# Performance work log

Measured on AMD Instinct MI355X. Metric: run time of the kernel, lower is better.

Reference implementation:

```python
import jax, jax.numpy as jnp
import numpy as np

CENTER_EXTEND_PX = 3.0  # center_extend_px
SIGMA = 2.0             # center_gt_blur
KSIZE = 21              # GaussianLayer: ReflectionPad2d(10) + 21x21 depthwise gaussian
PAD = KSIZE // 2


def _gaussian_kernel():
    ax = np.arange(KSIZE, dtype=np.float64) - PAD
    xx, yy = np.meshgrid(ax, ax)
    g = np.exp(-(xx ** 2 + yy ** 2) / (2.0 * SIGMA ** 2))
    g /= g.sum()
    return jnp.asarray(g, dtype=jnp.float32)


def _blur(x, kernel):
    # x: [H, W]; reflect-pad then VALID depthwise conv == GaussianLayer
    xp = jnp.pad(x, PAD, mode='reflect')
    return jax.lax.conv_general_dilated(xp[None, None], kernel[None, None], (1, 1), 'VALID')[0, 0]


def setup_inputs():
    key = jax.random.key(0)
    B, N, H, W = 4, 64, 512, 512
    kc = jax.random.fold_in(key, 1)
    # centers[b, n] = (y, x) pixel coordinates; >0 means valid
    centers = jax.random.randint(kc, (B, N, 2), 1, min(H, W)).astype(jnp.float32)
    centerdir_gt = jnp.zeros((B, 6, H, W), dtype=jnp.float32)
    return {"centers": centers, "centerdir_gt": centerdir_gt, "kernel": _gaussian_kernel()}


def reference(centers, centerdir_gt, kernel):
    B, _, H, W = centerdir_gt.shape
    # xym grid: xym[0] varies along width, xym[1] varies along height (integer coords)
    grid_h = jnp.arange(H, dtype=jnp.float32)[:, None]  # xym[1]: [H,1]
    grid_w = jnp.arange(W, dtype=jnp.float32)[None, :]  # xym[0]: [1,W]

    def per_item(c, gt_b):
        valid = (c[:, 0] > 0) | (c[:, 1] > 0)          # [N]
        cy, cx = c[:, 0], c[:, 1]
        # original: X = xym[1] (height grid) paired with center_x = centers[:,1]
        dx = grid_h[:, :, None] - cx                    # [H,1,N]
        dy = grid_w[:, :, None] - cy                    # [1,W,N]
        d2 = dx * dx + dy * dy                          # [H,W,N]; squared dist (same argmin as sqrt)
        d2 = jnp.where(valid[None, None, :], d2, jnp.inf)
        ids = jnp.argmin(d2, axis=-1)                   # [H,W] nearest valid center per pixel
        gt_X = cx[ids] - grid_h                         # [H,W]
        gt_Y = cy[ids] - grid_w
        r2 = gt_X * gt_X + gt_Y * gt_Y
        gt_R = jnp.where(r2 > 0, jnp.sqrt(jnp.where(r2 > 0, r2, 1.0)), 0.0)
        gt_theta = jnp.arctan2(gt_Y, jnp.where(r2 > 0, gt_X, 1.0))  # atan2(0,1)=0 == atan2(0,0)
        s, co = jnp.sin(gt_theta), jnp.cos(gt_theta)
        M = jnp.sqrt(s * s + co * co)
        s, co = s / M, co / M
        near = (jnp.abs(gt_X) < CENTER_EXTEND_PX) & (jnp.abs(gt_Y) < CENTER_EXTEND_PX)
        has_valid = valid.any()
        mask0 = jnp.where(has_valid, near.astype(jnp.float32), 0.0)  # == 1 - gt_center_mask
        blurred = _blur(mask0, kernel)
        m = blurred.max()
        center_mask = jnp.where(mask0.max() > 0, blurred / jnp.maximum(m, 1e-12), 0.0)
        ch = jnp.where(has_valid, jnp.stack([gt_R, gt_theta, s, co]), gt_b[:4])
        return jnp.concatenate([ch, gt_b[4:5], center_mask[None]], axis=0)  # [6,H,W]

    return jax.vmap(per_item)(centers, centerdir_gt)
```

## Files before the change

### kernel.cpp

```cpp
#include <hip/hip_runtime.h>
#include <math.h>
#include <limits.h>

namespace {
constexpr int BB   = 4;
constexpr int NCH  = 6;
constexpr int HH   = 512;
constexpr int WW   = 512;
constexpr int NCEN = 64;
constexpr int KSZ  = 21;
constexpr int PADR = 10;
constexpr int HW   = HH * WW;
constexpr int SENT = -1024;

__device__ __forceinline__ int refl(int q, int n) {
    q = (q < 0) ? -q : q;
    q = (q >= n) ? (2 * n - 2 - q) : q;
    return q;
}

__global__ __launch_bounds__(256) void k_geom(
    const float* __restrict__ centers,
    const float* __restrict__ gt,
    float* __restrict__ out,
    float* __restrict__ mask)
{
    __shared__ int2  s_cen[2][NCEN];
    __shared__ float s_cxf[NCEN], s_cyf[NCEN];
    __shared__ int   s_has;

    const int b   = blockIdx.y;
    const int tid = threadIdx.x;
    const int r0  = blockIdx.x * 2;

    if (tid == 0) s_has = 0;
    __syncthreads();
    if (tid < NCEN) {
        float cy = centers[(b * NCEN + tid) * 2 + 0];
        float cx = centers[(b * NCEN + tid) * 2 + 1];
        bool valid = (cy > 0.0f) || (cx > 0.0f);
        if (valid) atomicOr(&s_has, 1);
        s_cyf[tid] = cy;
        s_cxf[tid] = cx;
        int icx = valid ? (int)cx : SENT;
        int icy = valid ? (int)cy : SENT;
        int dx0 = r0 - icx;
        int dx1 = r0 + 1 - icx;
        s_cen[0][tid] = make_int2(icy * 8, 64 * dx0 * dx0 + tid);
        s_cen[1][tid] = make_int2(icy * 8, 64 * dx1 * dx1 + tid);
    }
    __syncthreads();

    const int rr  = tid >> 7;
    const int w0  = (tid & 127) * 4;
    const int row = r0 + rr;
    const int idx0 = row * WW + w0;

    const int iw8_0 = (w0 + 0) * 8;
    const int iw8_1 = (w0 + 1) * 8;
    const int iw8_2 = (w0 + 2) * 8;
    const int iw8_3 = (w0 + 3) * 8;
    int b0 = INT_MAX, b1 = INT_MAX, b2 = INT_MAX, b3 = INT_MAX;

    const int2* cen = s_cen[rr];
#pragma unroll 8
    for (int i = 0; i < NCEN; ++i) {
        int2 c = cen[i];
        int d0 = iw8_0 - c.x; b0 = min(b0, __mul24(d0, d0) + c.y);
        int d1 = iw8_1 - c.x; b1 = min(b1, __mul24(d1, d1) + c.y);
        int d2 = iw8_2 - c.x; b2 = min(b2, __mul24(d2, d2) + c.y);
        int d3 = iw8_3 - c.x; b3 = min(b3, __mul24(d3, d3) + c.y);
    }
    int bi[4] = { b0 & 63, b1 & 63, b2 & 63, b3 & 63 };

    const bool hv = (s_has != 0);
    float aR[4], aT[4], aS[4], aC[4], aM[4];
    const float fh = (float)row;
#pragma unroll
    for (int j = 0; j < 4; ++j) {
        float cxw = s_cxf[bi[j]];
        float cyw = s_cyf[bi[j]];
        float gX = cxw - fh;
        float gY = cyw - (float)(w0 + j);
        float r2 = gX * gX + gY * gY;
        bool rpos = r2 > 0.0f;
        float R = rpos ? sqrtf(r2) : 0.0f;
        aR[j] = R;
        aT[j] = atan2f(gY, rpos ? gX : 1.0f);
        float invR = rpos ? (1.0f / R) : 0.0f;
        aS[j] = rpos ? gY * invR : 0.0f;
        aC[j] = rpos ? gX * invR : 1.0f;
        bool nearc = (fabsf(gX) < 3.0f) && (fabsf(gY) < 3.0f);
        aM[j] = (hv && nearc) ? 1.0f : 0.0f;
    }

    const size_t base = (size_t)b * NCH * HW + (size_t)idx0;
    if (hv) {
        *(float4*)&out[base + 0 * (size_t)HW] = make_float4(aR[0], aR[1], aR[2], aR[3]);
        *(float4*)&out[base + 1 * (size_t)HW] = make_float4(aT[0], aT[1], aT[2], aT[3]);
        *(float4*)&out[base + 2 * (size_t)HW] = make_float4(aS[0], aS[1], aS[2], aS[3]);
        *(float4*)&out[base + 3 * (size_t)HW] = make_float4(aC[0], aC[1], aC[2], aC[3]);
    } else {
        *(float4*)&out[base + 0 * (size_t)HW] = *(const float4*)&gt[base + 0 * (size_t)HW];
        *(float4*)&out[base + 1 * (size_t)HW] = *(const float4*)&gt[base + 1 * (size_t)HW];
        *(float4*)&out[base + 2 * (size_t)HW] = *(const float4*)&gt[base + 2 * (size_t)HW];
        *(float4*)&out[base + 3 * (size_t)HW] = *(const float4*)&gt[base + 3 * (size_t)HW];
    }
    *(float4*)&out[base + 4 * (size_t)HW] = *(const float4*)&gt[base + 4 * (size_t)HW];
    *(float4*)&out[base + 5 * (size_t)HW] = make_float4(0.f, 0.f, 0.f, 0.f);
    *(float4*)&mask[(size_t)b * HW + idx0] = make_float4(aM[0], aM[1], aM[2], aM[3]);
}

__device__ __forceinline__ void load_k1(const float* __restrict__ g2d, float* k1) {
    if (threadIdx.x < KSZ) {
        float s = 0.0f;
#pragma unroll
        for (int j = 0; j < KSZ; ++j) s += g2d[threadIdx.x * KSZ + j];
        k1[threadIdx.x] = s;
    }
}

__device__ __forceinline__ void vpass(const float* __restrict__ mb,
                                      const float* __restrict__ k1,
                                      float* __restrict__ tmp,
                                      int rA, int nh, int cLo, int nwT) {
    for (int e = threadIdx.x; e < nh * nwT; e += 256) {
        int lr = e / nwT;
        int c  = cLo + (e - lr * nwT);
        int r  = rA + lr;
        float acc = 0.0f;
#pragma unroll
        for (int dv = -PADR; dv <= PADR; ++dv) {
            int q = refl(r + dv, HH);
            acc = fmaf(k1[dv + PADR], mb[q * WW + c], acc);
        }
        tmp[lr * 46 + (c - cLo)] = acc;
    }
}

__global__ __launch_bounds__(256) void k_blur_sparse(
    const float* __restrict__ centers,
    const float* __restrict__ mask,
    const float* __restrict__ g2d,
    unsigned int* __restrict__ maxbuf)
{
    const int b  = blockIdx.y;
    const int ci = blockIdx.x;
    float cy = centers[(b * NCEN + ci) * 2 + 0];
    float cx = centers[(b * NCEN + ci) * 2 + 1];
    if (!((cy > 0.0f) || (cx > 0.0f))) return;
    int icx = (int)cx, icy = (int)cy;
    int rA = max(icx - 12, 0), rB = min(icx + 12, HH - 1);
    int cA = max(icy - 12, 0), cB = min(icy + 12, WW - 1);
    int cLo = max(cA - PADR, 0), cHi = min(cB + PADR, WW - 1);
    int nh = rB - rA + 1, nw = cB - cA + 1, nwT = cHi - cLo + 1;

    __shared__ float k1[KSZ];
    __shared__ float tmp[25 * 46];
    load_k1(g2d, k1);
    __syncthreads();
    vpass(mask + (size_t)b * HW, k1, tmp, rA, nh, cLo, nwT);
    __syncthreads();

    float vmax = 0.0f;
    for (int e = threadIdx.x; e < nh * nw; e += 256) {
        int lr = e / nw;
        int w  = cA + (e - lr * nw);
        float acc = 0.0f;
#pragma unroll
        for (int d = -PADR; d <= PADR; ++d) {
            int q = refl(w + d, WW);
            acc = fmaf(k1[d + PADR], tmp[lr * 46 + (q - cLo)], acc);
        }
        vmax = fmaxf(vmax, acc);
    }
#pragma unroll
    for (int off = 32; off > 0; off >>= 1)
        vmax = fmaxf(vmax, __shfl_down(vmax, off, 64));
    __shared__ float swr[4];
    const int lane = threadIdx.x & 63, wid = threadIdx.x >> 6;
    if (lane == 0) swr[wid] = vmax;
    __syncthreads();
    if (threadIdx.x == 0) {
        float m = fmaxf(fmaxf(swr[0], swr[1]), fmaxf(swr[2], swr[3]));
        atomicMax(&maxbuf[b], __float_as_uint(m));
    }
}

__global__ __launch_bounds__(256) void k_norm_sparse(
    const float* __restrict__ centers,
    const float* __restrict__ mask,
    const float* __restrict__ g2d,
    const unsigned int* __restrict__ maxbuf,
    float* __restrict__ out)
{
    const int b  = blockIdx.y;
    const int ci = blockIdx.x;
    float cy = centers[(b * NCEN + ci) * 2 + 0];
    float cx = centers[(b * NCEN + ci) * 2 + 1];
    if (!((cy > 0.0f) || (cx > 0.0f))) return;
    int icx = (int)cx, icy = (int)cy;
    int rA = max(icx - 12, 0), rB = min(icx + 12, HH - 1);
    int cA = max(icy - 12, 0), cB = min(icy + 12, WW - 1);
    int cLo = max(cA - PADR, 0), cHi = min(cB + PADR, WW - 1);
    int nh = rB - rA + 1, nw = cB - cA + 1, nwT = cHi - cLo + 1;

    __shared__ float k1[KSZ];
    __shared__ float tmp[25 * 46];
    load_k1(g2d, k1);
    __syncthreads();
    vpass(mask + (size_t)b * HW, k1, tmp, rA, nh, cLo, nwT);
    __syncthreads();

    const float inv = 1.0f / fmaxf(__uint_as_float(maxbuf[b]), 1e-12f);
    float* o5 = out + ((size_t)b * NCH + 5) * HW;
    for (int e = threadIdx.x; e < nh * nw; e += 256) {
        int lr = e / nw;
        int w  = cA + (e - lr * nw);
        float acc = 0.0f;
#pragma unroll
        for (int d = -PADR; d <= PADR; ++d) {
            int q = refl(w + d, WW);
            acc = fmaf(k1[d + PADR], tmp[lr * 46 + (q - cLo)], acc);
        }
        o5[(rA + lr) * WW + w] = acc * inv;
    }
}

}

extern "C" void kernel_launch(void* const* d_in, const int* in_sizes, int n_in,
                              void* d_out, int out_size, void* d_ws, size_t ws_size,
                              hipStream_t stream) {
    (void)in_sizes; (void)n_in; (void)out_size; (void)ws_size;
    const float* centers = (const float*)d_in[0];
    const float* gt      = (const float*)d_in[1];
    const float* g2d     = (const float*)d_in[2];
    float* out  = (float*)d_out;
    float* mask = (float*)d_ws;
    unsigned int* maxbuf = (unsigned int*)((char*)d_ws + (size_t)BB * HW * sizeof(float));

    hipMemsetAsync(maxbuf, 0, BB * sizeof(unsigned int), stream);
    dim3 gridG(HW / 1024, BB);
    k_geom<<<gridG, 256, 0, stream>>>(centers, gt, out, mask);
    dim3 gridS(NCEN, BB);
    k_blur_sparse<<<gridS, 256, 0, stream>>>(centers, mask, g2d, maxbuf);
    k_norm_sparse<<<gridS, 256, 0, stream>>>(centers, mask, g2d, maxbuf, out);
}
```

Baseline: 110.3 us.

## Cache blurred boxes in workspace, stage mask patch in LDS, drop memset

The blur kernel now stores each center's blurred 25x25 box in a workspace buffer, so the normalize kernel only scales and scatters it instead of repeating both blur passes. The mask patch is loaded into shared memory before the vertical pass, replacing strided global reads. The maxbuf reset moves into the geometry kernel, which removes the separate memset launch. The cost is extra workspace and more LDS per block. Overall time is likely dominated by the full-image geometry kernel, so the sparse-kernel savings may be small.

```diff
diff --git a/kernel.cpp b/kernel.cpp
--- a/kernel.cpp
+++ b/kernel.cpp
@@ -12,6 +12,7 @@
 constexpr int PADR = 10;
 constexpr int HW   = HH * WW;
 constexpr int SENT = -1024;
+constexpr int BOXSTRIDE = 640;
 
 __device__ __forceinline__ int refl(int q, int n) {
     q = (q < 0) ? -q : q;
@@ -23,7 +24,8 @@
     const float* __restrict__ centers,
     const float* __restrict__ gt,
     float* __restrict__ out,
-    float* __restrict__ mask)
+    float* __restrict__ mask,
+    unsigned int* __restrict__ maxbuf)
 {
     __shared__ int2  s_cen[2][NCEN];
     __shared__ float s_cxf[NCEN], s_cyf[NCEN];
@@ -33,6 +35,7 @@
     const int tid = threadIdx.x;
     const int r0  = blockIdx.x * 2;
 
+    if (blockIdx.x == 0 && tid == 0) maxbuf[b] = 0u;
     if (tid == 0) s_has = 0;
     __syncthreads();
     if (tid < NCEN) {
@@ -120,28 +123,11 @@
     }
 }
 
-__device__ __forceinline__ void vpass(const float* __restrict__ mb,
-                                      const float* __restrict__ k1,
-                                      float* __restrict__ tmp,
-                                      int rA, int nh, int cLo, int nwT) {
-    for (int e = threadIdx.x; e < nh * nwT; e += 256) {
-        int lr = e / nwT;
-        int c  = cLo + (e - lr * nwT);
-        int r  = rA + lr;
-        float acc = 0.0f;
-#pragma unroll
-        for (int dv = -PADR; dv <= PADR; ++dv) {
-            int q = refl(r + dv, HH);
-            acc = fmaf(k1[dv + PADR], mb[q * WW + c], acc);
-        }
-        tmp[lr * 46 + (c - cLo)] = acc;
-    }
-}
-
 __global__ __launch_bounds__(256) void k_blur_sparse(
     const float* __restrict__ centers,
     const float* __restrict__ mask,
     const float* __restrict__ g2d,
+    float* __restrict__ blurbox,
     unsigned int* __restrict__ maxbuf)
 {
     const int b  = blockIdx.y;
@@ -149,29 +135,51 @@
     float cy = centers[(b * NCEN + ci) * 2 + 0];
     float cx = centers[(b * NCEN + ci) * 2 + 1];
     if (!((cy > 0.0f) || (cx > 0.0f))) return;
-    int icx = (int)cx, icy = (int)cy;
-    int rA = max(icx - 12, 0), rB = min(icx + 12, HH - 1);
-    int cA = max(icy - 12, 0), cB = min(icy + 12, WW - 1);
-    int cLo = max(cA - PADR, 0), cHi = min(cB + PADR, WW - 1);
-    int nh = rB - rA + 1, nw = cB - cA + 1, nwT = cHi - cLo + 1;
+    const int icx = (int)cx, icy = (int)cy;
+    const int rA = max(icx - 12, 0), rB = min(icx + 12, HH - 1);
+    const int cA = max(icy - 12, 0), cB = min(icy + 12, WW - 1);
+    const int pr0 = max(rA - PADR, 0), pr1 = min(rB + PADR, HH - 1);
+    const int pc0 = max(cA - PADR, 0), pc1 = min(cB + PADR, WW - 1);
+    const int nr = pr1 - pr0 + 1, nc = pc1 - pc0 + 1;
+    const int nh = rB - rA + 1,  nw = cB - cA + 1;
 
     __shared__ float k1[KSZ];
+    __shared__ float patch[45 * 48];
     __shared__ float tmp[25 * 46];
     load_k1(g2d, k1);
-    __syncthreads();
-    vpass(mask + (size_t)b * HW, k1, tmp, rA, nh, cLo, nwT);
+
+    const float* mb = mask + (size_t)b * HW;
+    for (int e = threadIdx.x; e < nr * nc; e += 256) {
+        int r = e / nc, c = e - r * nc;
+        patch[r * 48 + c] = mb[(pr0 + r) * WW + (pc0 + c)];
+    }
+    __syncthreads();
+
+    for (int e = threadIdx.x; e < nh * nc; e += 256) {
+        int lr = e / nc, j = e - lr * nc;
+        int r  = rA + lr;
+        float acc = 0.0f;
+#pragma unroll
+        for (int dv = -PADR; dv <= PADR; ++dv) {
+            int q = refl(r + dv, HH);
+            acc = fmaf(k1[dv + PADR], patch[(q - pr0) * 48 + j], acc);
+        }
+        tmp[lr * 46 + j] = acc;
+    }
     __syncthreads();
 
     float vmax = 0.0f;
+    float* bx = blurbox + (size_t)(b * NCEN + ci) * BOXSTRIDE;
     for (int e = threadIdx.x; e < nh * nw; e += 256) {
-        int lr = e / nw;
-        int w  = cA + (e - lr * nw);
+        int lr = e / nw, j = e - lr * nw;
+        int w  = cA + j;
         float acc = 0.0f;
 #pragma unroll
         for (int d = -PADR; d <= PADR; ++d) {
             int q = refl(w + d, WW);
-            acc = fmaf(k1[d + PADR], tmp[lr * 46 + (q - cLo)], acc);
+            acc = fmaf(k1[d + PADR], tmp[lr * 46 + (q - pc0)], acc);
         }
+        bx[lr * 25 + j] = acc;
         vmax = fmaxf(vmax, acc);
     }
 #pragma unroll
@@ -189,8 +197,7 @@
 
 __global__ __launch_bounds__(256) void k_norm_sparse(
     const float* __restrict__ centers,
-    const float* __restrict__ mask,
-    const float* __restrict__ g2d,
+    const float* __restrict__ blurbox,
     const unsigned int* __restrict__ maxbuf,
     float* __restrict__ out)
 {
@@ -199,31 +206,17 @@
     float cy = centers[(b * NCEN + ci) * 2 + 0];
     float cx = centers[(b * NCEN + ci) * 2 + 1];
     if (!((cy > 0.0f) || (cx > 0.0f))) return;
-    int icx = (int)cx, icy = (int)cy;
-    int rA = max(icx - 12, 0), rB = min(icx + 12, HH - 1);
-    int cA = max(icy - 12, 0), cB = min(icy + 12, WW - 1);
-    int cLo = max(cA - PADR, 0), cHi = min(cB + PADR, WW - 1);
-    int nh = rB - rA + 1, nw = cB - cA + 1, nwT = cHi - cLo + 1;
-
-    __shared__ float k1[KSZ];
-    __shared__ float tmp[25 * 46];
-    load_k1(g2d, k1);
-    __syncthreads();
-    vpass(mask + (size_t)b * HW, k1, tmp, rA, nh, cLo, nwT);
-    __syncthreads();
+    const int icx = (int)cx, icy = (int)cy;
+    const int rA = max(icx - 12, 0), rB = min(icx + 12, HH - 1);
+    const int cA = max(icy - 12, 0), cB = min(icy + 12, WW - 1);
+    const int nh = rB - rA + 1, nw = cB - cA + 1;
 
     const float inv = 1.0f / fmaxf(__uint_as_float(maxbuf[b]), 1e-12f);
+    const float* bx = blurbox + (size_t)(b * NCEN + ci) * BOXSTRIDE;
     float* o5 = out + ((size_t)b * NCH + 5) * HW;
     for (int e = threadIdx.x; e < nh * nw; e += 256) {
-        int lr = e / nw;
-        int w  = cA + (e - lr * nw);
-        float acc = 0.0f;
-#pragma unroll
-        for (int d = -PADR; d <= PADR; ++d) {
-            int q = refl(w + d, WW);
-            acc = fmaf(k1[d + PADR], tmp[lr * 46 + (q - cLo)], acc);
-        }
-        o5[(rA + lr) * WW + w] = acc * inv;
+        int lr = e / nw, j = e - lr * nw;
+        o5[(rA + lr) * WW + (cA + j)] = bx[lr * 25 + j] * inv;
     }
 }
 
@@ -238,12 +231,13 @@
     const float* g2d     = (const float*)d_in[2];
     float* out  = (float*)d_out;
     float* mask = (float*)d_ws;
-    unsigned int* maxbuf = (unsigned int*)((char*)d_ws + (size_t)BB * HW * sizeof(float));
-
-    hipMemsetAsync(maxbuf, 0, BB * sizeof(unsigned int), stream);
+    float* blurbox = (float*)d_ws + (size_t)BB * HW;
+    unsigned int* maxbuf =
+        (unsigned int*)((float*)d_ws + (size_t)BB * HW + (size_t)BB * NCEN * BOXSTRIDE);
+
     dim3 gridG(HW / 1024, BB);
-    k_geom<<<gridG, 256, 0, stream>>>(centers, gt, out, mask);
+    k_geom<<<gridG, 256, 0, stream>>>(centers, gt, out, mask, maxbuf);
     dim3 gridS(NCEN, BB);
-    k_blur_sparse<<<gridS, 256, 0, stream>>>(centers, mask, g2d, maxbuf);
-    k_norm_sparse<<<gridS, 256, 0, stream>>>(centers, mask, g2d, maxbuf, out);
-}
+    k_blur_sparse<<<gridS, 256, 0, stream>>>(centers, mask, g2d, blurbox, maxbuf);
+    k_norm_sparse<<<gridS, 256, 0, stream>>>(centers, blurbox, maxbuf, out);
+}
```

Result: faster. 99.00 us (-10.3%).
